# Kernel optimization log

Hardware: AMD Instinct MI355X
Metric: run time of the kernel (lower is better)

The kernel has to match this reference:

```python
import jax, jax.numpy as jnp
import numpy as np

NUM_HEADS = 8

def setup_inputs() -> dict:
    key = jax.random.key(0)
    ks = jax.random.split(key, 9)
    b, s, d = 2, 2048, 512
    e = d * NUM_HEADS  # 4096
    sc = 0.02
    return {
        "x": jax.random.normal(ks[0], (b, s, d), jnp.float32),
        "Wq": jax.random.normal(ks[1], (e, d), jnp.float32) * sc,
        "bq": jax.random.normal(ks[2], (e,), jnp.float32) * sc,
        "Wk": jax.random.normal(ks[3], (e, d), jnp.float32) * sc,
        "bk": jax.random.normal(ks[4], (e,), jnp.float32) * sc,
        "Wv": jax.random.normal(ks[5], (e, d), jnp.float32) * sc,
        "bv": jax.random.normal(ks[6], (e,), jnp.float32) * sc,
        "Wo": jax.random.normal(ks[7], (d, e), jnp.float32) * sc,
        "bo": jax.random.normal(ks[8], (d,), jnp.float32) * sc,
    }

def reference(x, Wq, bq, Wk, bk, Wv, bv, Wo, bo):
    b, s, d = x.shape
    h = NUM_HEADS
    hd = d  # head_dim == model_dimension in this module
    # QKV projections: [b, s, h*hd]
    q = (x @ Wq.T + bq).reshape(b, s, h, hd)
    k = (x @ Wk.T + bk).reshape(b, s, h, hd)
    v = (x @ Wv.T + bv).reshape(b, s, h, hd)
    # scores: [b, h, s_q, s_k]
    scores = jnp.einsum("bqhd,bkhd->bhqk", q, k) / jnp.sqrt(jnp.float32(hd))
    attn = jax.nn.softmax(scores, axis=-1)
    ctx = jnp.einsum("bhqk,bkhd->bqhd", attn, v).reshape(b, s, h * hd)
    return ctx @ Wo.T + bo
```

## Files before the change

kernel.cpp:

```cpp
#include <hip/hip_runtime.h>
#include <hip/hip_bf16.h>

typedef __hip_bfloat16 bf16t;
typedef short bf16x8 __attribute__((ext_vector_type(8)));
typedef float f32x4 __attribute__((ext_vector_type(4)));

__device__ __forceinline__ float b2f(short s) {
    unsigned u = ((unsigned)(unsigned short)s) << 16;
    float f;
    __builtin_memcpy(&f, &u, 4);
    return f;
}

__device__ __forceinline__ unsigned short f2b(float f) {
    unsigned u;
    __builtin_memcpy(&u, &f, 4);
    unsigned r = (u + 0x7fffu + ((u >> 16) & 1u)) >> 16;
    return (unsigned short)r;
}

__device__ __forceinline__ void gload_lds16(const void* g, void* l) {
    __builtin_amdgcn_global_load_lds(
        (const __attribute__((address_space(1))) void*)g,
        (__attribute__((address_space(3))) void*)l,
        16, 0, 0);
}

template<int EPI>
__global__ __launch_bounds__(512, 2)
void gemm8p(const bf16t* __restrict__ Ag, const bf16t* __restrict__ Bg,
            void* __restrict__ Cg, const float* __restrict__ bias,
            float* __restrict__ part,
            int K, int lda, int ldb, int ldc,
            long aOffB, long aOffH, long bOffB, long bOffH,
            long cOffB, long cOffH, float scale)
{
    __shared__ __align__(16) char lds8[131072];

    unsigned gx = gridDim.x, gy = gridDim.y;
    unsigned nwg = gx * gy * gridDim.z;
    unsigned wg = (blockIdx.z * gy + blockIdx.y) * gx + blockIdx.x;
    if ((nwg & 7u) == 0u) wg = (wg & 7u) * (nwg >> 3) + (wg >> 3);
    const unsigned pz = wg / (gx * gy);
    const unsigned prem = wg - pz * gx * gy;
    const unsigned py = prem / gx;
    const unsigned px = prem - py * gx;

    const int zb = pz >> 3, zh = pz & 7;
    const int brow = py * 256;
    const int bcol = px * 256;

    const size_t ldab = (size_t)lda * 2;
    const size_t ldbb = (size_t)ldb * 2;
    const char* Agb = (const char*)(Ag + (size_t)zb * aOffB + (size_t)zh * aOffH)
                      + (size_t)brow * ldab;
    const char* Bgb = (const char*)(Bg + (size_t)zb * bOffB + (size_t)zh * bOffH)
                      + (size_t)bcol * ldbb;

    const int t    = threadIdx.x;
    const int lane = t & 63;
    const int wid  = t >> 6;
    const int wm   = wid >> 2;
    const int wn   = wid & 3;
    const int lr   = lane & 15;
    const int lk   = lane >> 4;

    const int srow = t >> 2;
    const int scg  = (t & 3) ^ ((srow >> 1) & 3);
    const size_t aSrc = (size_t)srow * ldab + (size_t)scg * 16;
    const size_t bSrc = (size_t)srow * ldbb + (size_t)scg * 16;
    const int dst0 = t * 16;
    char* ldsA = lds8;
    char* ldsB = lds8 + 65536;

    const int rchunk = lk ^ ((lr >> 1) & 3);
    const int aByte = (wm * 128 + lr) * 64 + rchunk * 16;
    const int bByte = (wn * 64 + lr) * 64 + rchunk * 16;

    f32x4 acc[8][4];
#pragma unroll
    for (int i = 0; i < 8; ++i)
#pragma unroll
        for (int j = 0; j < 4; ++j)
            acc[i][j] = (f32x4){0.f, 0.f, 0.f, 0.f};

    const int nk = K >> 5;

#define STAGE_A(kt, bufi) do {                                              \
        const char* s_ = Agb + (size_t)(kt) * 64 + aSrc;                    \
        char* d_ = ldsA + (bufi) * 16384 + dst0;                            \
        gload_lds16(s_, d_);                                                \
        gload_lds16(s_ + 128 * ldab, d_ + 8192);                            \
    } while (0)
#define STAGE_B(kt, bufi) do {                                              \
        const char* s_ = Bgb + (size_t)(kt) * 64 + bSrc;                    \
        char* d_ = ldsB + (bufi) * 16384 + dst0;                            \
        gload_lds16(s_, d_);                                                \
        gload_lds16(s_ + 128 * ldbb, d_ + 8192);                            \
    } while (0)

    const int npro = nk < 3 ? nk : 3;
    for (int p = 0; p < npro; ++p) { STAGE_A(p, p & 3); STAGE_B(p, p & 3); }
    if (npro == 3) asm volatile("s_waitcnt vmcnt(8)" ::: "memory");
    else           asm volatile("s_waitcnt vmcnt(0)" ::: "memory");
    __builtin_amdgcn_s_barrier();

    for (int kt = 0; kt < nk; ++kt) {
        const int buf  = kt & 3;
        const int bufS = (kt + 3) & 3;
        const bool st  = (kt + 3) < nk;
        const char* lA = ldsA + buf * 16384;
        const char* lB = ldsB + buf * 16384;

        bf16x8 af[4], bfv[4];
#pragma unroll
        for (int i = 0; i < 4; ++i) af[i]  = *(const bf16x8*)(lA + aByte + i * 1024);
#pragma unroll
        for (int j = 0; j < 4; ++j) bfv[j] = *(const bf16x8*)(lB + bByte + j * 1024);
        if (st) STAGE_A(kt + 3, bufS);
        __builtin_amdgcn_s_setprio(1);
#pragma unroll
        for (int i = 0; i < 4; ++i)
#pragma unroll
            for (int j = 0; j < 4; ++j)
                acc[i][j] = __builtin_amdgcn_mfma_f32_16x16x32_bf16(af[i], bfv[j], acc[i][j], 0, 0, 0);
        __builtin_amdgcn_s_setprio(0);
        asm volatile("" ::: "memory");
        __builtin_amdgcn_s_barrier();

        bf16x8 af2[4];
#pragma unroll
        for (int i = 0; i < 4; ++i) af2[i] = *(const bf16x8*)(lA + aByte + (i + 4) * 1024);
        if (st) STAGE_B(kt + 3, bufS);
        if (st)                  asm volatile("s_waitcnt vmcnt(8)" ::: "memory");
        else if (kt + 2 < nk)    asm volatile("s_waitcnt vmcnt(4)" ::: "memory");
        else if (kt + 1 < nk)    asm volatile("s_waitcnt vmcnt(0)" ::: "memory");
        __builtin_amdgcn_s_setprio(1);
#pragma unroll
        for (int i = 0; i < 4; ++i)
#pragma unroll
            for (int j = 0; j < 4; ++j)
                acc[i + 4][j] = __builtin_amdgcn_mfma_f32_16x16x32_bf16(af2[i], bfv[j], acc[i + 4][j], 0, 0, 0);
        __builtin_amdgcn_s_setprio(0);
        asm volatile("" ::: "memory");
        __builtin_amdgcn_s_barrier();
    }
#undef STAGE_A
#undef STAGE_B

    if (EPI == 4) {
#pragma unroll
        for (int i = 0; i < 8; ++i)
#pragma unroll
            for (int j = 0; j < 4; ++j)
#pragma unroll
                for (int r = 0; r < 4; ++r)
                    acc[i][j][r] = __expf(acc[i][j][r] * scale);
#pragma unroll
        for (int i = 0; i < 8; ++i)
#pragma unroll
            for (int r = 0; r < 4; ++r) {
                float v = acc[i][0][r] + acc[i][1][r] + acc[i][2][r] + acc[i][3][r];
                v += __shfl_xor(v, 1);
                v += __shfl_xor(v, 2);
                v += __shfl_xor(v, 4);
                v += __shfl_xor(v, 8);
                if (lr == 0)
                    part[((size_t)pz * 2048 + brow + wm * 128 + i * 16 + lk * 4 + r) * 32
                         + px * 4 + wn] = v;
            }
        __syncthreads();
        unsigned short* lC = (unsigned short*)lds8;
#pragma unroll
        for (int i = 0; i < 8; ++i)
#pragma unroll
            for (int j = 0; j < 4; ++j) {
                int col = wn * 64 + j * 16 + lr;
#pragma unroll
                for (int r = 0; r < 4; ++r) {
                    int row = wm * 128 + i * 16 + lk * 4 + r;
                    lC[row * 256 + col] = f2b(acc[i][j][r]);
                }
            }
        __syncthreads();
        unsigned short* C = (unsigned short*)((bf16t*)Cg + (size_t)zb * cOffB + (size_t)zh * cOffH);
#pragma unroll
        for (int p = 0; p < 16; ++p) {
            int c  = p * 512 + t;
            int row = c >> 5;
            int cc  = c & 31;
            bf16x8 v = *(const bf16x8*)(lC + (size_t)c * 8);
            *(bf16x8*)(C + (size_t)(brow + row) * ldc + bcol + cc * 8) = v;
        }
    } else if (EPI == 3) {
        __syncthreads();
        float* ldsInv = (float*)lds8;
        if (t < 256) {
            const float* pp = part + ((size_t)pz * 2048 + brow + t) * 32;
            float s = 0.f;
#pragma unroll
            for (int p = 0; p < 32; ++p) s += pp[p];
            ldsInv[t] = 1.0f / s;
        }
        __syncthreads();
        float linv[8][4];
#pragma unroll
        for (int i = 0; i < 8; ++i)
#pragma unroll
            for (int r = 0; r < 4; ++r)
                linv[i][r] = ldsInv[wm * 128 + i * 16 + lk * 4 + r];
        __syncthreads();
        unsigned short* lC = (unsigned short*)lds8;
#pragma unroll
        for (int i = 0; i < 8; ++i)
#pragma unroll
            for (int j = 0; j < 4; ++j) {
                int col = wn * 64 + j * 16 + lr;
#pragma unroll
                for (int r = 0; r < 4; ++r) {
                    int row = wm * 128 + i * 16 + lk * 4 + r;
                    lC[row * 256 + col] = f2b(acc[i][j][r] * linv[i][r]);
                }
            }
        __syncthreads();
        unsigned short* C = (unsigned short*)((bf16t*)Cg + (size_t)zb * cOffB + (size_t)zh * cOffH);
#pragma unroll
        for (int p = 0; p < 16; ++p) {
            int c  = p * 512 + t;
            int row = c >> 5;
            int cc  = c & 31;
            bf16x8 v = *(const bf16x8*)(lC + (size_t)c * 8);
            *(bf16x8*)(C + (size_t)(brow + row) * ldc + bcol + cc * 8) = v;
        }
    } else if (EPI == 0) {
        __syncthreads();
        unsigned short* lC = (unsigned short*)lds8;
#pragma unroll
        for (int i = 0; i < 8; ++i)
#pragma unroll
            for (int j = 0; j < 4; ++j) {
                int col = wn * 64 + j * 16 + lr;
                float badd = bias ? bias[bcol + col] : 0.f;
#pragma unroll
                for (int r = 0; r < 4; ++r) {
                    int row = wm * 128 + i * 16 + lk * 4 + r;
                    lC[row * 256 + col] = f2b(acc[i][j][r] * scale + badd);
                }
            }
        __syncthreads();
        unsigned short* C = (unsigned short*)((bf16t*)Cg + (size_t)zb * cOffB + (size_t)zh * cOffH);
#pragma unroll
        for (int p = 0; p < 16; ++p) {
            int c  = p * 512 + t;
            int row = c >> 5;
            int cc  = c & 31;
            bf16x8 v = *(const bf16x8*)(lC + (size_t)c * 8);
            *(bf16x8*)(C + (size_t)(brow + row) * ldc + bcol + cc * 8) = v;
        }
    } else {
        unsigned short* C = (unsigned short*)Cg;
#pragma unroll
        for (int i = 0; i < 8; ++i)
#pragma unroll
            for (int j = 0; j < 4; ++j) {
                int col = bcol + wn * 64 + j * 16 + lr;
                int hh = col >> 9, dd = col & 511;
                float badd = bias ? bias[col] : 0.f;
                int row0 = brow + wm * 128 + i * 16 + lk * 4;
                int bb = row0 >> 11, ss0 = row0 & 2047;
                ushort4 pack;
                pack.x = f2b(acc[i][j][0] * scale + badd);
                pack.y = f2b(acc[i][j][1] * scale + badd);
                pack.z = f2b(acc[i][j][2] * scale + badd);
                pack.w = f2b(acc[i][j][3] * scale + badd);
                size_t addr = ((((size_t)(bb * 8 + hh)) * 512 + dd) << 11) + (size_t)ss0;
                *(ushort4*)(C + addr) = pack;
            }
    }
}

__global__ __launch_bounds__(256, 3)
void gemm_of32(const bf16t* __restrict__ Ag, const bf16t* __restrict__ Bg,
               float* __restrict__ Cg, const float* __restrict__ bias,
               int K, int lda, int ldb, int ldc)
{
    __shared__ __align__(16) char lds[49152];

    unsigned gx = gridDim.x, gy = gridDim.y;
    unsigned nwg = gx * gy;
    unsigned wg = blockIdx.y * gx + blockIdx.x;
    if ((nwg & 7u) == 0u) wg = (wg & 7u) * (nwg >> 3) + (wg >> 3);
    const unsigned py = wg / gx;
    const unsigned px = wg - py * gx;
    const int brow = py * 128;
    const int bcol = px * 64;

    const int t    = threadIdx.x;
    const int lane = t & 63;
    const int wid  = t >> 6;
    const int wr   = wid >> 1, wc = wid & 1;
    const int lr   = lane & 15;
    const int lk   = lane >> 4;

    const size_t ldab = (size_t)lda * 2;
    const size_t ldbb = (size_t)ldb * 2;
    const char* Agb = (const char*)Ag + (size_t)brow * ldab;
    const char* Bgb = (const char*)Bg + (size_t)bcol * ldbb;

    const int srow = t >> 2;
    const int scg  = (t & 3) ^ ((srow >> 1) & 3);
    const size_t aSrc = (size_t)srow * ldab + (size_t)scg * 16;
    const size_t bSrc = (size_t)srow * ldbb + (size_t)scg * 16;
    char* ldsA = lds;
    char* ldsB = lds + 32768;

    const int rchunk = lk ^ ((lr >> 1) & 3);
    const int aByte = (wr * 64 + lr) * 64 + rchunk * 16;
    const int bByte = (wc * 32 + lr) * 64 + rchunk * 16;

    f32x4 acc[4][2];
#pragma unroll
    for (int i = 0; i < 4; ++i)
#pragma unroll
        for (int j = 0; j < 2; ++j)
            acc[i][j] = (f32x4){0.f, 0.f, 0.f, 0.f};

    const int nk = K >> 5;

#define STAGE_O(kt, bufi) do {                                              \
        const char* sa_ = Agb + (size_t)(kt) * 64 + aSrc;                   \
        gload_lds16(sa_,             ldsA + (bufi) * 8192 + t * 16);        \
        gload_lds16(sa_ + 64 * ldab, ldsA + (bufi) * 8192 + 4096 + t * 16); \
        gload_lds16(Bgb + (size_t)(kt) * 64 + bSrc,                         \
                    ldsB + (bufi) * 4096 + t * 16);                         \
    } while (0)

    for (int p = 0; p < 3; ++p) STAGE_O(p, p);
    asm volatile("s_waitcnt vmcnt(6)" ::: "memory");
    __builtin_amdgcn_s_barrier();

    for (int kt = 0; kt < nk; ++kt) {
        const int buf  = kt & 3;
        const bool st  = (kt + 3) < nk;
        const char* lA = ldsA + buf * 8192;
        const char* lB = ldsB + buf * 4096;

        bf16x8 af[4], bfv[2];
#pragma unroll
        for (int i = 0; i < 4; ++i) af[i]  = *(const bf16x8*)(lA + aByte + i * 1024);
#pragma unroll
        for (int j = 0; j < 2; ++j) bfv[j] = *(const bf16x8*)(lB + bByte + j * 1024);
        if (st) STAGE_O(kt + 3, (kt + 3) & 3);
        if (st)                  asm volatile("s_waitcnt vmcnt(6)" ::: "memory");
        else if (kt + 2 < nk)    asm volatile("s_waitcnt vmcnt(3)" ::: "memory");
        else if (kt + 1 < nk)    asm volatile("s_waitcnt vmcnt(0)" ::: "memory");
        __builtin_amdgcn_s_setprio(1);
#pragma unroll
        for (int i = 0; i < 4; ++i)
#pragma unroll
            for (int j = 0; j < 2; ++j)
                acc[i][j] = __builtin_amdgcn_mfma_f32_16x16x32_bf16(af[i], bfv[j], acc[i][j], 0, 0, 0);
        __builtin_amdgcn_s_setprio(0);
        asm volatile("" ::: "memory");
        __builtin_amdgcn_s_barrier();
    }
#undef STAGE_O

    const int orow = brow + wr * 64;
    const int ocol = bcol + wc * 32;
#pragma unroll
    for (int i = 0; i < 4; ++i)
#pragma unroll
        for (int j = 0; j < 2; ++j) {
            int col = ocol + j * 16 + lr;
            float badd = bias[col];
#pragma unroll
            for (int r = 0; r < 4; ++r) {
                int row = orow + i * 16 + lk * 4 + r;
                Cg[(size_t)row * ldc + col] = acc[i][j][r] + badd;
            }
        }
}

__global__ __launch_bounds__(256)
void cvt5(const float* __restrict__ s0, const float* __restrict__ s1,
          const float* __restrict__ s2, const float* __restrict__ s3,
          const float* __restrict__ s4,
          bf16t* __restrict__ d0, bf16t* __restrict__ d1,
          bf16t* __restrict__ d2, bf16t* __restrict__ d3,
          bf16t* __restrict__ d4)
{
    const float* s;
    bf16t* d;
    switch (blockIdx.y) {
        case 0: s = s0; d = d0; break;
        case 1: s = s1; d = d1; break;
        case 2: s = s2; d = d2; break;
        case 3: s = s3; d = d3; break;
        default: s = s4; d = d4; break;
    }
    int i = blockIdx.x * 256 + threadIdx.x;
    float4 f = ((const float4*)s)[i];
    ushort4 o;
    o.x = f2b(f.x); o.y = f2b(f.y); o.z = f2b(f.z); o.w = f2b(f.w);
    ((ushort4*)d)[i] = o;
}

extern "C" void kernel_launch(void* const* d_in, const int* in_sizes, int n_in,
                              void* d_out, int out_size, void* d_ws, size_t ws_size,
                              hipStream_t stream)
{
    const float* x  = (const float*)d_in[0];
    const float* Wq = (const float*)d_in[1];
    const float* bq = (const float*)d_in[2];
    const float* Wk = (const float*)d_in[3];
    const float* bk = (const float*)d_in[4];
    const float* Wv = (const float*)d_in[5];
    const float* bv = (const float*)d_in[6];
    const float* Wo = (const float*)d_in[7];
    const float* bo = (const float*)d_in[8];

    const int Bn = 2, Sn = 2048, Dn = 512, Hn = 8, En = 4096;
    const int Mn = Bn * Sn;
    const float scl = 0.044194173824159216f;

    bf16t* base = (bf16t*)d_ws;
    size_t off = 0;
    bf16t* Qb  = base + off; off += (size_t)Mn * En;
    bf16t* Kb  = base + off; off += (size_t)Mn * En;
    bf16t* Vt  = base + off; off += (size_t)Mn * En;
    bf16t* Xb  = base + off; off += (size_t)Mn * Dn;
    bf16t* Wqb = base + off; off += (size_t)En * Dn;
    bf16t* Wkb = base + off; off += (size_t)En * Dn;
    bf16t* Wvb = base + off; off += (size_t)En * Dn;
    bf16t* Wob = base + off; off += (size_t)Dn * En;
    float* Pt  = (float*)(base + off); off += (size_t)16 * Sn * 32 * 2;
    bf16t* Sb  = base + off;

    cvt5<<<dim3(2048, 5, 1), 256, 0, stream>>>(x, Wq, Wk, Wv, Wo,
                                               Xb, Wqb, Wkb, Wvb, Wob);

    gemm8p<0><<<dim3(En / 256, Mn / 256, 1), 512, 0, stream>>>(
        Xb, Wqb, Qb, bq, nullptr, Dn, Dn, Dn, En, 0, 0, 0, 0, 0, 0, 1.0f);
    gemm8p<0><<<dim3(En / 256, Mn / 256, 1), 512, 0, stream>>>(
        Xb, Wkb, Kb, bk, nullptr, Dn, Dn, Dn, En, 0, 0, 0, 0, 0, 0, 1.0f);
    gemm8p<2><<<dim3(En / 256, Mn / 256, 1), 512, 0, stream>>>(
        Xb, Wvb, Vt, bv, nullptr, Dn, Dn, Dn, En, 0, 0, 0, 0, 0, 0, 1.0f);

    gemm8p<4><<<dim3(Sn / 256, Sn / 256, 16), 512, 0, stream>>>(
        Qb, Kb, Sb, nullptr, Pt, Dn, En, En, Sn,
        (long)Sn * En, (long)Dn, (long)Sn * En, (long)Dn,
        (long)Hn * Sn * Sn, (long)Sn * Sn, scl);

    gemm8p<3><<<dim3(Dn / 256, Sn / 256, 16), 512, 0, stream>>>(
        Sb, Vt, Qb, nullptr, Pt, Sn, Sn, Sn, En,
        (long)Hn * Sn * Sn, (long)Sn * Sn, (long)Hn * Dn * Sn, (long)Dn * Sn,
        (long)Sn * En, (long)Dn, 1.0f);

    gemm_of32<<<dim3(Dn / 64, Mn / 128, 1), 256, 0, stream>>>(
        Qb, Wob, (float*)d_out, bo, En, En, En, Dn);
}
```

Baseline: 300.0 us.

## Shrink GEMM tile to 128x256 with triple-buffered LDS for higher occupancy

Halves the M dimension of the main GEMM block tile from 256 to 128 and cuts the LDS pipeline from four stages to three, shrinking shared memory from 128KB to 72KB. Launch bounds are raised to allow more blocks per CU. The k-loop is restructured into a single MFMA phase per step with an extra barrier and lgkmcnt wait before compute, and the same barrier is added to the output-projection GEMM. This aims to improve occupancy and latency hiding at the cost of less data reuse per tile, more global traffic on the B operand, and an added barrier per iteration.

```diff
diff --git a/kernel.cpp b/kernel.cpp
--- a/kernel.cpp
+++ b/kernel.cpp
@@ -27,15 +27,15 @@
 }
 
 template<int EPI>
-__global__ __launch_bounds__(512, 2)
-void gemm8p(const bf16t* __restrict__ Ag, const bf16t* __restrict__ Bg,
+__global__ __launch_bounds__(512, 4)
+void gemm3b(const bf16t* __restrict__ Ag, const bf16t* __restrict__ Bg,
             void* __restrict__ Cg, const float* __restrict__ bias,
             float* __restrict__ part,
             int K, int lda, int ldb, int ldc,
             long aOffB, long aOffH, long bOffB, long bOffH,
             long cOffB, long cOffH, float scale)
 {
-    __shared__ __align__(16) char lds8[131072];
+    __shared__ __align__(16) char lds8[73728];
 
     unsigned gx = gridDim.x, gy = gridDim.y;
     unsigned nwg = gx * gy * gridDim.z;
@@ -47,7 +47,7 @@
     const unsigned px = prem - py * gx;
 
     const int zb = pz >> 3, zh = pz & 7;
-    const int brow = py * 256;
+    const int brow = py * 128;
     const int bcol = px * 256;
 
     const size_t ldab = (size_t)lda * 2;
@@ -69,55 +69,58 @@
     const int scg  = (t & 3) ^ ((srow >> 1) & 3);
     const size_t aSrc = (size_t)srow * ldab + (size_t)scg * 16;
     const size_t bSrc = (size_t)srow * ldbb + (size_t)scg * 16;
-    const int dst0 = t * 16;
     char* ldsA = lds8;
-    char* ldsB = lds8 + 65536;
+    char* ldsB = lds8 + 24576;
 
     const int rchunk = lk ^ ((lr >> 1) & 3);
-    const int aByte = (wm * 128 + lr) * 64 + rchunk * 16;
+    const int aByte = (wm * 64 + lr) * 64 + rchunk * 16;
     const int bByte = (wn * 64 + lr) * 64 + rchunk * 16;
 
-    f32x4 acc[8][4];
-#pragma unroll
-    for (int i = 0; i < 8; ++i)
+    f32x4 acc[4][4];
+#pragma unroll
+    for (int i = 0; i < 4; ++i)
 #pragma unroll
         for (int j = 0; j < 4; ++j)
             acc[i][j] = (f32x4){0.f, 0.f, 0.f, 0.f};
 
     const int nk = K >> 5;
 
-#define STAGE_A(kt, bufi) do {                                              \
-        const char* s_ = Agb + (size_t)(kt) * 64 + aSrc;                    \
-        char* d_ = ldsA + (bufi) * 16384 + dst0;                            \
-        gload_lds16(s_, d_);                                                \
-        gload_lds16(s_ + 128 * ldab, d_ + 8192);                            \
+#define STAGE(kt, bufi) do {                                                \
+        const char* sa_ = Agb + (size_t)(kt) * 64 + aSrc;                   \
+        gload_lds16(sa_, ldsA + (bufi) * 8192 + t * 16);                    \
+        const char* sb_ = Bgb + (size_t)(kt) * 64 + bSrc;                   \
+        gload_lds16(sb_,              ldsB + (bufi) * 16384 + t * 16);      \
+        gload_lds16(sb_ + 128 * ldbb, ldsB + (bufi) * 16384 + 8192 + t * 16);\
     } while (0)
-#define STAGE_B(kt, bufi) do {                                              \
-        const char* s_ = Bgb + (size_t)(kt) * 64 + bSrc;                    \
-        char* d_ = ldsB + (bufi) * 16384 + dst0;                            \
-        gload_lds16(s_, d_);                                                \
-        gload_lds16(s_ + 128 * ldbb, d_ + 8192);                            \
-    } while (0)
-
-    const int npro = nk < 3 ? nk : 3;
-    for (int p = 0; p < npro; ++p) { STAGE_A(p, p & 3); STAGE_B(p, p & 3); }
-    if (npro == 3) asm volatile("s_waitcnt vmcnt(8)" ::: "memory");
-    else           asm volatile("s_waitcnt vmcnt(0)" ::: "memory");
+
+    STAGE(0, 0);
+    if (nk > 1) {
+        STAGE(1, 1);
+        asm volatile("s_waitcnt vmcnt(3)" ::: "memory");
+    } else {
+        asm volatile("s_waitcnt vmcnt(0)" ::: "memory");
+    }
     __builtin_amdgcn_s_barrier();
 
+    int bufR = 0, bufS = 2;
     for (int kt = 0; kt < nk; ++kt) {
-        const int buf  = kt & 3;
-        const int bufS = (kt + 3) & 3;
-        const bool st  = (kt + 3) < nk;
-        const char* lA = ldsA + buf * 16384;
-        const char* lB = ldsB + buf * 16384;
+        const char* lA = ldsA + bufR * 8192;
+        const char* lB = ldsB + bufR * 16384;
 
         bf16x8 af[4], bfv[4];
 #pragma unroll
         for (int i = 0; i < 4; ++i) af[i]  = *(const bf16x8*)(lA + aByte + i * 1024);
 #pragma unroll
         for (int j = 0; j < 4; ++j) bfv[j] = *(const bf16x8*)(lB + bByte + j * 1024);
-        if (st) STAGE_A(kt + 3, bufS);
+
+        if (kt + 2 < nk) {
+            STAGE(kt + 2, bufS);
+            asm volatile("s_waitcnt vmcnt(3)" ::: "memory");
+        } else if (kt + 1 < nk) {
+            asm volatile("s_waitcnt vmcnt(0)" ::: "memory");
+        }
+        __builtin_amdgcn_s_barrier();
+        asm volatile("s_waitcnt lgkmcnt(0)" ::: "memory");
         __builtin_amdgcn_s_setprio(1);
 #pragma unroll
         for (int i = 0; i < 4; ++i)
@@ -128,36 +131,21 @@
         asm volatile("" ::: "memory");
         __builtin_amdgcn_s_barrier();
 
-        bf16x8 af2[4];
-#pragma unroll
-        for (int i = 0; i < 4; ++i) af2[i] = *(const bf16x8*)(lA + aByte + (i + 4) * 1024);
-        if (st) STAGE_B(kt + 3, bufS);
-        if (st)                  asm volatile("s_waitcnt vmcnt(8)" ::: "memory");
-        else if (kt + 2 < nk)    asm volatile("s_waitcnt vmcnt(4)" ::: "memory");
-        else if (kt + 1 < nk)    asm volatile("s_waitcnt vmcnt(0)" ::: "memory");
-        __builtin_amdgcn_s_setprio(1);
-#pragma unroll
-        for (int i = 0; i < 4; ++i)
-#pragma unroll
-            for (int j = 0; j < 4; ++j)
-                acc[i + 4][j] = __builtin_amdgcn_mfma_f32_16x16x32_bf16(af2[i], bfv[j], acc[i + 4][j], 0, 0, 0);
-        __builtin_amdgcn_s_setprio(0);
-        asm volatile("" ::: "memory");
-        __builtin_amdgcn_s_barrier();
+        bufR = (bufR == 2) ? 0 : bufR + 1;
+        bufS = (bufS == 2) ? 0 : bufS + 1;
     }
-#undef STAGE_A
-#undef STAGE_B
+#undef STAGE
 
     if (EPI == 4) {
 #pragma unroll
-        for (int i = 0; i < 8; ++i)
+        for (int i = 0; i < 4; ++i)
 #pragma unroll
             for (int j = 0; j < 4; ++j)
 #pragma unroll
                 for (int r = 0; r < 4; ++r)
                     acc[i][j][r] = __expf(acc[i][j][r] * scale);
 #pragma unroll
-        for (int i = 0; i < 8; ++i)
+        for (int i = 0; i < 4; ++i)
 #pragma unroll
             for (int r = 0; r < 4; ++r) {
                 float v = acc[i][0][r] + acc[i][1][r] + acc[i][2][r] + acc[i][3][r];
@@ -166,26 +154,26 @@
                 v += __shfl_xor(v, 4);
                 v += __shfl_xor(v, 8);
                 if (lr == 0)
-                    part[((size_t)pz * 2048 + brow + wm * 128 + i * 16 + lk * 4 + r) * 32
+                    part[((size_t)pz * 2048 + brow + wm * 64 + i * 16 + lk * 4 + r) * 32
                          + px * 4 + wn] = v;
             }
         __syncthreads();
         unsigned short* lC = (unsigned short*)lds8;
 #pragma unroll
-        for (int i = 0; i < 8; ++i)
+        for (int i = 0; i < 4; ++i)
 #pragma unroll
             for (int j = 0; j < 4; ++j) {
                 int col = wn * 64 + j * 16 + lr;
 #pragma unroll
                 for (int r = 0; r < 4; ++r) {
-                    int row = wm * 128 + i * 16 + lk * 4 + r;
+                    int row = wm * 64 + i * 16 + lk * 4 + r;
                     lC[row * 256 + col] = f2b(acc[i][j][r]);
                 }
             }
         __syncthreads();
         unsigned short* C = (unsigned short*)((bf16t*)Cg + (size_t)zb * cOffB + (size_t)zh * cOffH);
 #pragma unroll
-        for (int p = 0; p < 16; ++p) {
+        for (int p = 0; p < 8; ++p) {
             int c  = p * 512 + t;
             int row = c >> 5;
             int cc  = c & 31;
@@ -195,7 +183,7 @@
     } else if (EPI == 3) {
         __syncthreads();
         float* ldsInv = (float*)lds8;
-        if (t < 256) {
+        if (t < 128) {
             const float* pp = part + ((size_t)pz * 2048 + brow + t) * 32;
             float s = 0.f;
 #pragma unroll
@@ -203,29 +191,29 @@
             ldsInv[t] = 1.0f / s;
         }
         __syncthreads();
-        float linv[8][4];
-#pragma unroll
-        for (int i = 0; i < 8; ++i)
+        float linv[4][4];
+#pragma unroll
+        for (int i = 0; i < 4; ++i)
 #pragma unroll
             for (int r = 0; r < 4; ++r)
-                linv[i][r] = ldsInv[wm * 128 + i * 16 + lk * 4 + r];
+                linv[i][r] = ldsInv[wm * 64 + i * 16 + lk * 4 + r];
         __syncthreads();
         unsigned short* lC = (unsigned short*)lds8;
 #pragma unroll
-        for (int i = 0; i < 8; ++i)
+        for (int i = 0; i < 4; ++i)
 #pragma unroll
             for (int j = 0; j < 4; ++j) {
                 int col = wn * 64 + j * 16 + lr;
 #pragma unroll
                 for (int r = 0; r < 4; ++r) {
-                    int row = wm * 128 + i * 16 + lk * 4 + r;
+                    int row = wm * 64 + i * 16 + lk * 4 + r;
                     lC[row * 256 + col] = f2b(acc[i][j][r] * linv[i][r]);
                 }
             }
         __syncthreads();
         unsigned short* C = (unsigned short*)((bf16t*)Cg + (size_t)zb * cOffB + (size_t)zh * cOffH);
 #pragma unroll
-        for (int p = 0; p < 16; ++p) {
+        for (int p = 0; p < 8; ++p) {
             int c  = p * 512 + t;
             int row = c >> 5;
             int cc  = c & 31;
@@ -236,21 +224,21 @@
         __syncthreads();
         unsigned short* lC = (unsigned short*)lds8;
 #pragma unroll
-        for (int i = 0; i < 8; ++i)
+        for (int i = 0; i < 4; ++i)
 #pragma unroll
             for (int j = 0; j < 4; ++j) {
                 int col = wn * 64 + j * 16 + lr;
                 float badd = bias ? bias[bcol + col] : 0.f;
 #pragma unroll
                 for (int r = 0; r < 4; ++r) {
-                    int row = wm * 128 + i * 16 + lk * 4 + r;
+                    int row = wm * 64 + i * 16 + lk * 4 + r;
                     lC[row * 256 + col] = f2b(acc[i][j][r] * scale + badd);
                 }
             }
         __syncthreads();
         unsigned short* C = (unsigned short*)((bf16t*)Cg + (size_t)zb * cOffB + (size_t)zh * cOffH);
 #pragma unroll
-        for (int p = 0; p < 16; ++p) {
+        for (int p = 0; p < 8; ++p) {
             int c  = p * 512 + t;
             int row = c >> 5;
             int cc  = c & 31;
@@ -260,13 +248,13 @@
     } else {
         unsigned short* C = (unsigned short*)Cg;
 #pragma unroll
-        for (int i = 0; i < 8; ++i)
+        for (int i = 0; i < 4; ++i)
 #pragma unroll
             for (int j = 0; j < 4; ++j) {
                 int col = bcol + wn * 64 + j * 16 + lr;
                 int hh = col >> 9, dd = col & 511;
                 float badd = bias ? bias[col] : 0.f;
-                int row0 = brow + wm * 128 + i * 16 + lk * 4;
+                int row0 = brow + wm * 64 + i * 16 + lk * 4;
                 int bb = row0 >> 11, ss0 = row0 & 2047;
                 ushort4 pack;
                 pack.x = f2b(acc[i][j][0] * scale + badd);
@@ -354,6 +342,8 @@
         if (st)                  asm volatile("s_waitcnt vmcnt(6)" ::: "memory");
         else if (kt + 2 < nk)    asm volatile("s_waitcnt vmcnt(3)" ::: "memory");
         else if (kt + 1 < nk)    asm volatile("s_waitcnt vmcnt(0)" ::: "memory");
+        __builtin_amdgcn_s_barrier();
+        asm volatile("s_waitcnt lgkmcnt(0)" ::: "memory");
         __builtin_amdgcn_s_setprio(1);
 #pragma unroll
         for (int i = 0; i < 4; ++i)
@@ -440,19 +430,19 @@
     cvt5<<<dim3(2048, 5, 1), 256, 0, stream>>>(x, Wq, Wk, Wv, Wo,
                                                Xb, Wqb, Wkb, Wvb, Wob);
 
-    gemm8p<0><<<dim3(En / 256, Mn / 256, 1), 512, 0, stream>>>(
+    gemm3b<0><<<dim3(En / 256, Mn / 128, 1), 512, 0, stream>>>(
         Xb, Wqb, Qb, bq, nullptr, Dn, Dn, Dn, En, 0, 0, 0, 0, 0, 0, 1.0f);
-    gemm8p<0><<<dim3(En / 256, Mn / 256, 1), 512, 0, stream>>>(
+    gemm3b<0><<<dim3(En / 256, Mn / 128, 1), 512, 0, stream>>>(
         Xb, Wkb, Kb, bk, nullptr, Dn, Dn, Dn, En, 0, 0, 0, 0, 0, 0, 1.0f);
-    gemm8p<2><<<dim3(En / 256, Mn / 256, 1), 512, 0, stream>>>(
+    gemm3b<2><<<dim3(En / 256, Mn / 128, 1), 512, 0, stream>>>(
         Xb, Wvb, Vt, bv, nullptr, Dn, Dn, Dn, En, 0, 0, 0, 0, 0, 0, 1.0f);
 
-    gemm8p<4><<<dim3(Sn / 256, Sn / 256, 16), 512, 0, stream>>>(
+    gemm3b<4><<<dim3(Sn / 256, Sn / 128, 16), 512, 0, stream>>>(
         Qb, Kb, Sb, nullptr, Pt, Dn, En, En, Sn,
         (long)Sn * En, (long)Dn, (long)Sn * En, (long)Dn,
         (long)Hn * Sn * Sn, (long)Sn * Sn, scl);
 
-    gemm8p<3><<<dim3(Dn / 256, Sn / 256, 16), 512, 0, stream>>>(
+    gemm3b<3><<<dim3(Dn / 256, Sn / 128, 16), 512, 0, stream>>>(
         Sb, Vt, Qb, nullptr, Pt, Sn, Sn, Sn, En,
         (long)Hn * Sn * Sn, (long)Sn * Sn, (long)Hn * Dn * Sn, (long)Dn * Sn,
         (long)Sn * En, (long)Dn, 1.0f);
```

Result: slower. 307.0 us (+2.3%).

## Fuse QKV projections into one GEMM and restage main loop with two-deep prefetch

Applied to the files above, without the earlier changes.

The three separate Q/K/V projection GEMMs are merged into a single launch over a concatenated weight buffer. A new epilogue routes each column block to Q, K or the transposed V layout, and the biases are packed into one buffer by the conversion kernel. The GEMM main loop is restructured to process two k-tiles per iteration with a prefetch distance of two instead of three, adding extra barriers and lgkmcnt waits before each MFMA block. This cuts launch count and improves wave fill for the projection, but the shallower prefetch and extra barriers may expose more memory latency.

```diff
diff --git a/kernel.cpp b/kernel.cpp
--- a/kernel.cpp
+++ b/kernel.cpp
@@ -28,7 +28,7 @@
 
 template<int EPI>
 __global__ __launch_bounds__(512, 2)
-void gemm8p(const bf16t* __restrict__ Ag, const bf16t* __restrict__ Bg,
+void gemm4p(const bf16t* __restrict__ Ag, const bf16t* __restrict__ Bg,
             void* __restrict__ Cg, const float* __restrict__ bias,
             float* __restrict__ part,
             int K, int lda, int ldb, int ldc,
@@ -99,25 +99,31 @@
         gload_lds16(s_ + 128 * ldbb, d_ + 8192);                            \
     } while (0)
 
-    const int npro = nk < 3 ? nk : 3;
-    for (int p = 0; p < npro; ++p) { STAGE_A(p, p & 3); STAGE_B(p, p & 3); }
-    if (npro == 3) asm volatile("s_waitcnt vmcnt(8)" ::: "memory");
-    else           asm volatile("s_waitcnt vmcnt(0)" ::: "memory");
+    STAGE_A(0, 0); STAGE_B(0, 0);
+    STAGE_A(1, 1); STAGE_B(1, 1);
+    asm volatile("s_waitcnt vmcnt(4)" ::: "memory");
     __builtin_amdgcn_s_barrier();
 
-    for (int kt = 0; kt < nk; ++kt) {
-        const int buf  = kt & 3;
-        const int bufS = (kt + 3) & 3;
-        const bool st  = (kt + 3) < nk;
-        const char* lA = ldsA + buf * 16384;
-        const char* lB = ldsB + buf * 16384;
+    const int nh = nk >> 1;
+    for (int J = 0; J < nh; ++J) {
+        const int t0 = 2 * J;
+        const int b0 = t0 & 3, b1 = (t0 + 1) & 3;
+        const int s0 = t0 + 2, s1 = t0 + 3;
+        const bool st = s0 < nk;
+        const int sb0 = s0 & 3, sb1 = s1 & 3;
+        const char* lA0 = ldsA + b0 * 16384;
+        const char* lB0 = ldsB + b0 * 16384;
+        const char* lA1 = ldsA + b1 * 16384;
+        const char* lB1 = ldsB + b1 * 16384;
 
         bf16x8 af[4], bfv[4];
 #pragma unroll
-        for (int i = 0; i < 4; ++i) af[i]  = *(const bf16x8*)(lA + aByte + i * 1024);
-#pragma unroll
-        for (int j = 0; j < 4; ++j) bfv[j] = *(const bf16x8*)(lB + bByte + j * 1024);
-        if (st) STAGE_A(kt + 3, bufS);
+        for (int i = 0; i < 4; ++i) af[i]  = *(const bf16x8*)(lA0 + aByte + i * 1024);
+#pragma unroll
+        for (int j = 0; j < 4; ++j) bfv[j] = *(const bf16x8*)(lB0 + bByte + j * 1024);
+        if (st) STAGE_A(s0, sb0);
+        __builtin_amdgcn_s_barrier();
+        asm volatile("s_waitcnt lgkmcnt(0)" ::: "memory");
         __builtin_amdgcn_s_setprio(1);
 #pragma unroll
         for (int i = 0; i < 4; ++i)
@@ -130,11 +136,45 @@
 
         bf16x8 af2[4];
 #pragma unroll
-        for (int i = 0; i < 4; ++i) af2[i] = *(const bf16x8*)(lA + aByte + (i + 4) * 1024);
-        if (st) STAGE_B(kt + 3, bufS);
-        if (st)                  asm volatile("s_waitcnt vmcnt(8)" ::: "memory");
-        else if (kt + 2 < nk)    asm volatile("s_waitcnt vmcnt(4)" ::: "memory");
-        else if (kt + 1 < nk)    asm volatile("s_waitcnt vmcnt(0)" ::: "memory");
+        for (int i = 0; i < 4; ++i) af2[i] = *(const bf16x8*)(lA0 + aByte + (i + 4) * 1024);
+        if (st) STAGE_B(s0, sb0);
+        if (st) asm volatile("s_waitcnt vmcnt(4)" ::: "memory");
+        else    asm volatile("s_waitcnt vmcnt(0)" ::: "memory");
+        __builtin_amdgcn_s_barrier();
+        asm volatile("s_waitcnt lgkmcnt(0)" ::: "memory");
+        __builtin_amdgcn_s_setprio(1);
+#pragma unroll
+        for (int i = 0; i < 4; ++i)
+#pragma unroll
+            for (int j = 0; j < 4; ++j)
+                acc[i + 4][j] = __builtin_amdgcn_mfma_f32_16x16x32_bf16(af2[i], bfv[j], acc[i + 4][j], 0, 0, 0);
+        __builtin_amdgcn_s_setprio(0);
+        asm volatile("" ::: "memory");
+        __builtin_amdgcn_s_barrier();
+
+#pragma unroll
+        for (int i = 0; i < 4; ++i) af[i]  = *(const bf16x8*)(lA1 + aByte + i * 1024);
+#pragma unroll
+        for (int j = 0; j < 4; ++j) bfv[j] = *(const bf16x8*)(lB1 + bByte + j * 1024);
+        if (st) STAGE_A(s1, sb1);
+        __builtin_amdgcn_s_barrier();
+        asm volatile("s_waitcnt lgkmcnt(0)" ::: "memory");
+        __builtin_amdgcn_s_setprio(1);
+#pragma unroll
+        for (int i = 0; i < 4; ++i)
+#pragma unroll
+            for (int j = 0; j < 4; ++j)
+                acc[i][j] = __builtin_amdgcn_mfma_f32_16x16x32_bf16(af[i], bfv[j], acc[i][j], 0, 0, 0);
+        __builtin_amdgcn_s_setprio(0);
+        asm volatile("" ::: "memory");
+        __builtin_amdgcn_s_barrier();
+
+#pragma unroll
+        for (int i = 0; i < 4; ++i) af2[i] = *(const bf16x8*)(lA1 + aByte + (i + 4) * 1024);
+        if (st) STAGE_B(s1, sb1);
+        if (st) asm volatile("s_waitcnt vmcnt(4)" ::: "memory");
+        __builtin_amdgcn_s_barrier();
+        asm volatile("s_waitcnt lgkmcnt(0)" ::: "memory");
         __builtin_amdgcn_s_setprio(1);
 #pragma unroll
         for (int i = 0; i < 4; ++i)
@@ -232,30 +272,53 @@
             bf16x8 v = *(const bf16x8*)(lC + (size_t)c * 8);
             *(bf16x8*)(C + (size_t)(brow + row) * ldc + bcol + cc * 8) = v;
         }
-    } else if (EPI == 0) {
-        __syncthreads();
-        unsigned short* lC = (unsigned short*)lds8;
-#pragma unroll
-        for (int i = 0; i < 8; ++i)
-#pragma unroll
-            for (int j = 0; j < 4; ++j) {
-                int col = wn * 64 + j * 16 + lr;
-                float badd = bias ? bias[bcol + col] : 0.f;
-#pragma unroll
-                for (int r = 0; r < 4; ++r) {
-                    int row = wm * 128 + i * 16 + lk * 4 + r;
-                    lC[row * 256 + col] = f2b(acc[i][j][r] * scale + badd);
+    } else if (EPI == 5) {
+        const int sel = bcol >> 12;
+        const int colw0 = bcol & 4095;
+        if (sel < 2) {
+            __syncthreads();
+            unsigned short* lC = (unsigned short*)lds8;
+#pragma unroll
+            for (int i = 0; i < 8; ++i)
+#pragma unroll
+                for (int j = 0; j < 4; ++j) {
+                    int col = wn * 64 + j * 16 + lr;
+                    float badd = bias[bcol + col];
+#pragma unroll
+                    for (int r = 0; r < 4; ++r) {
+                        int row = wm * 128 + i * 16 + lk * 4 + r;
+                        lC[row * 256 + col] = f2b(acc[i][j][r] + badd);
+                    }
                 }
+            __syncthreads();
+            unsigned short* C = (unsigned short*)((bf16t*)Cg + (size_t)sel * cOffB);
+#pragma unroll
+            for (int p = 0; p < 16; ++p) {
+                int c  = p * 512 + t;
+                int row = c >> 5;
+                int cc  = c & 31;
+                bf16x8 v = *(const bf16x8*)(lC + (size_t)c * 8);
+                *(bf16x8*)(C + (size_t)(brow + row) * ldc + colw0 + cc * 8) = v;
             }
-        __syncthreads();
-        unsigned short* C = (unsigned short*)((bf16t*)Cg + (size_t)zb * cOffB + (size_t)zh * cOffH);
-#pragma unroll
-        for (int p = 0; p < 16; ++p) {
-            int c  = p * 512 + t;
-            int row = c >> 5;
-            int cc  = c & 31;
-            bf16x8 v = *(const bf16x8*)(lC + (size_t)c * 8);
-            *(bf16x8*)(C + (size_t)(brow + row) * ldc + bcol + cc * 8) = v;
+        } else {
+            unsigned short* C = (unsigned short*)part;
+#pragma unroll
+            for (int i = 0; i < 8; ++i)
+#pragma unroll
+                for (int j = 0; j < 4; ++j) {
+                    int col = colw0 + wn * 64 + j * 16 + lr;
+                    int hh = col >> 9, dd = col & 511;
+                    float badd = bias[8192 + col];
+                    int row0 = brow + wm * 128 + i * 16 + lk * 4;
+                    int bb = row0 >> 11, ss0 = row0 & 2047;
+                    ushort4 pack;
+                    pack.x = f2b(acc[i][j][0] + badd);
+                    pack.y = f2b(acc[i][j][1] + badd);
+                    pack.z = f2b(acc[i][j][2] + badd);
+                    pack.w = f2b(acc[i][j][3] + badd);
+                    size_t addr = ((((size_t)(bb * 8 + hh)) * 512 + dd) << 11) + (size_t)ss0;
+                    *(ushort4*)(C + addr) = pack;
+                }
         }
     } else {
         unsigned short* C = (unsigned short*)Cg;
@@ -354,6 +417,8 @@
         if (st)                  asm volatile("s_waitcnt vmcnt(6)" ::: "memory");
         else if (kt + 2 < nk)    asm volatile("s_waitcnt vmcnt(3)" ::: "memory");
         else if (kt + 1 < nk)    asm volatile("s_waitcnt vmcnt(0)" ::: "memory");
+        __builtin_amdgcn_s_barrier();
+        asm volatile("s_waitcnt lgkmcnt(0)" ::: "memory");
         __builtin_amdgcn_s_setprio(1);
 #pragma unroll
         for (int i = 0; i < 4; ++i)
@@ -383,13 +448,25 @@
 }
 
 __global__ __launch_bounds__(256)
-void cvt5(const float* __restrict__ s0, const float* __restrict__ s1,
+void cvt6(const float* __restrict__ s0, const float* __restrict__ s1,
           const float* __restrict__ s2, const float* __restrict__ s3,
           const float* __restrict__ s4,
           bf16t* __restrict__ d0, bf16t* __restrict__ d1,
           bf16t* __restrict__ d2, bf16t* __restrict__ d3,
-          bf16t* __restrict__ d4)
+          bf16t* __restrict__ d4,
+          const float* __restrict__ bq, const float* __restrict__ bk,
+          const float* __restrict__ bv, float* __restrict__ bqkv)
 {
+    int i = blockIdx.x * 256 + threadIdx.x;
+    if (blockIdx.y == 5) {
+        if (i < 3072) {
+            int e = i * 4;
+            const float* src = (e < 4096) ? (bq + e) : (e < 8192) ? (bk + e - 4096) : (bv + e - 8192);
+            float4 f = *(const float4*)src;
+            *(float4*)(bqkv + e) = f;
+        }
+        return;
+    }
     const float* s;
     bf16t* d;
     switch (blockIdx.y) {
@@ -399,7 +476,6 @@
         case 3: s = s3; d = d3; break;
         default: s = s4; d = d4; break;
     }
-    int i = blockIdx.x * 256 + threadIdx.x;
     float4 f = ((const float4*)s)[i];
     ushort4 o;
     o.x = f2b(f.x); o.y = f2b(f.y); o.z = f2b(f.z); o.w = f2b(f.w);
@@ -430,29 +506,27 @@
     bf16t* Kb  = base + off; off += (size_t)Mn * En;
     bf16t* Vt  = base + off; off += (size_t)Mn * En;
     bf16t* Xb  = base + off; off += (size_t)Mn * Dn;
-    bf16t* Wqb = base + off; off += (size_t)En * Dn;
-    bf16t* Wkb = base + off; off += (size_t)En * Dn;
-    bf16t* Wvb = base + off; off += (size_t)En * Dn;
+    bf16t* Wc  = base + off; off += (size_t)3 * En * Dn;
     bf16t* Wob = base + off; off += (size_t)Dn * En;
+    float* Pbias = (float*)(base + off); off += 12288;
     float* Pt  = (float*)(base + off); off += (size_t)16 * Sn * 32 * 2;
     bf16t* Sb  = base + off;
 
-    cvt5<<<dim3(2048, 5, 1), 256, 0, stream>>>(x, Wq, Wk, Wv, Wo,
-                                               Xb, Wqb, Wkb, Wvb, Wob);
-
-    gemm8p<0><<<dim3(En / 256, Mn / 256, 1), 512, 0, stream>>>(
-        Xb, Wqb, Qb, bq, nullptr, Dn, Dn, Dn, En, 0, 0, 0, 0, 0, 0, 1.0f);
-    gemm8p<0><<<dim3(En / 256, Mn / 256, 1), 512, 0, stream>>>(
-        Xb, Wkb, Kb, bk, nullptr, Dn, Dn, Dn, En, 0, 0, 0, 0, 0, 0, 1.0f);
-    gemm8p<2><<<dim3(En / 256, Mn / 256, 1), 512, 0, stream>>>(
-        Xb, Wvb, Vt, bv, nullptr, Dn, Dn, Dn, En, 0, 0, 0, 0, 0, 0, 1.0f);
-
-    gemm8p<4><<<dim3(Sn / 256, Sn / 256, 16), 512, 0, stream>>>(
+    cvt6<<<dim3(2048, 6, 1), 256, 0, stream>>>(
+        x, Wq, Wk, Wv, Wo,
+        Xb, Wc, Wc + (size_t)En * Dn, Wc + (size_t)2 * En * Dn, Wob,
+        bq, bk, bv, Pbias);
+
+    gemm4p<5><<<dim3(3 * En / 256, Mn / 256, 1), 512, 0, stream>>>(
+        Xb, Wc, Qb, Pbias, (float*)Vt, Dn, Dn, Dn, En,
+        0, 0, 0, 0, (long)Mn * En, 0, 1.0f);
+
+    gemm4p<4><<<dim3(Sn / 256, Sn / 256, 16), 512, 0, stream>>>(
         Qb, Kb, Sb, nullptr, Pt, Dn, En, En, Sn,
         (long)Sn * En, (long)Dn, (long)Sn * En, (long)Dn,
         (long)Hn * Sn * Sn, (long)Sn * Sn, scl);
 
-    gemm8p<3><<<dim3(Dn / 256, Sn / 256, 16), 512, 0, stream>>>(
+    gemm4p<3><<<dim3(Dn / 256, Sn / 256, 16), 512, 0, stream>>>(
         Sb, Vt, Qb, nullptr, Pt, Sn, Sn, Sn, En,
         (long)Hn * Sn * Sn, (long)Sn * Sn, (long)Hn * Dn * Sn, (long)Dn * Sn,
         (long)Sn * En, (long)Dn, 1.0f);
```

New measurement: 296.7 us. Within noise of the previous version (-1.1%).

## Fuse Q/K/V projections into one GEMM launch and add pre-MFMA barriers

Applied to the files above, without the earlier changes.

Concatenates the bf16 Wq/Wk/Wv weights and their biases during conversion so that a single GEMM launch with a new epilogue computes all three projections. Column blocks are routed to Q, K (row-major through LDS) or transposed V depending on block column. This removes two kernel launches and the tail effects of three small grids. Separately, it inserts an s_barrier plus lgkmcnt(0) wait before each MFMA block in both GEMM main loops. These add synchronization that could cost throughput, or could act as a correctness/scheduling fix.

```diff
diff --git a/kernel.cpp b/kernel.cpp
--- a/kernel.cpp
+++ b/kernel.cpp
@@ -118,6 +118,8 @@
 #pragma unroll
         for (int j = 0; j < 4; ++j) bfv[j] = *(const bf16x8*)(lB + bByte + j * 1024);
         if (st) STAGE_A(kt + 3, bufS);
+        __builtin_amdgcn_s_barrier();
+        asm volatile("s_waitcnt lgkmcnt(0)" ::: "memory");
         __builtin_amdgcn_s_setprio(1);
 #pragma unroll
         for (int i = 0; i < 4; ++i)
@@ -135,6 +137,8 @@
         if (st)                  asm volatile("s_waitcnt vmcnt(8)" ::: "memory");
         else if (kt + 2 < nk)    asm volatile("s_waitcnt vmcnt(4)" ::: "memory");
         else if (kt + 1 < nk)    asm volatile("s_waitcnt vmcnt(0)" ::: "memory");
+        __builtin_amdgcn_s_barrier();
+        asm volatile("s_waitcnt lgkmcnt(0)" ::: "memory");
         __builtin_amdgcn_s_setprio(1);
 #pragma unroll
         for (int i = 0; i < 4; ++i)
@@ -232,30 +236,53 @@
             bf16x8 v = *(const bf16x8*)(lC + (size_t)c * 8);
             *(bf16x8*)(C + (size_t)(brow + row) * ldc + bcol + cc * 8) = v;
         }
-    } else if (EPI == 0) {
-        __syncthreads();
-        unsigned short* lC = (unsigned short*)lds8;
-#pragma unroll
-        for (int i = 0; i < 8; ++i)
-#pragma unroll
-            for (int j = 0; j < 4; ++j) {
-                int col = wn * 64 + j * 16 + lr;
-                float badd = bias ? bias[bcol + col] : 0.f;
-#pragma unroll
-                for (int r = 0; r < 4; ++r) {
-                    int row = wm * 128 + i * 16 + lk * 4 + r;
-                    lC[row * 256 + col] = f2b(acc[i][j][r] * scale + badd);
+    } else if (EPI == 5) {
+        const int sel = bcol >> 12;
+        const int colw0 = bcol & 4095;
+        if (sel < 2) {
+            __syncthreads();
+            unsigned short* lC = (unsigned short*)lds8;
+#pragma unroll
+            for (int i = 0; i < 8; ++i)
+#pragma unroll
+                for (int j = 0; j < 4; ++j) {
+                    int col = wn * 64 + j * 16 + lr;
+                    float badd = bias[bcol + col];
+#pragma unroll
+                    for (int r = 0; r < 4; ++r) {
+                        int row = wm * 128 + i * 16 + lk * 4 + r;
+                        lC[row * 256 + col] = f2b(acc[i][j][r] + badd);
+                    }
                 }
+            __syncthreads();
+            unsigned short* C = (unsigned short*)((bf16t*)Cg + (size_t)sel * cOffB);
+#pragma unroll
+            for (int p = 0; p < 16; ++p) {
+                int c  = p * 512 + t;
+                int row = c >> 5;
+                int cc  = c & 31;
+                bf16x8 v = *(const bf16x8*)(lC + (size_t)c * 8);
+                *(bf16x8*)(C + (size_t)(brow + row) * ldc + colw0 + cc * 8) = v;
             }
-        __syncthreads();
-        unsigned short* C = (unsigned short*)((bf16t*)Cg + (size_t)zb * cOffB + (size_t)zh * cOffH);
-#pragma unroll
-        for (int p = 0; p < 16; ++p) {
-            int c  = p * 512 + t;
-            int row = c >> 5;
-            int cc  = c & 31;
-            bf16x8 v = *(const bf16x8*)(lC + (size_t)c * 8);
-            *(bf16x8*)(C + (size_t)(brow + row) * ldc + bcol + cc * 8) = v;
+        } else {
+            unsigned short* C = (unsigned short*)part;
+#pragma unroll
+            for (int i = 0; i < 8; ++i)
+#pragma unroll
+                for (int j = 0; j < 4; ++j) {
+                    int col = colw0 + wn * 64 + j * 16 + lr;
+                    int hh = col >> 9, dd = col & 511;
+                    float badd = bias[8192 + col];
+                    int row0 = brow + wm * 128 + i * 16 + lk * 4;
+                    int bb = row0 >> 11, ss0 = row0 & 2047;
+                    ushort4 pack;
+                    pack.x = f2b(acc[i][j][0] + badd);
+                    pack.y = f2b(acc[i][j][1] + badd);
+                    pack.z = f2b(acc[i][j][2] + badd);
+                    pack.w = f2b(acc[i][j][3] + badd);
+                    size_t addr = ((((size_t)(bb * 8 + hh)) * 512 + dd) << 11) + (size_t)ss0;
+                    *(ushort4*)(C + addr) = pack;
+                }
         }
     } else {
         unsigned short* C = (unsigned short*)Cg;
@@ -354,6 +381,8 @@
         if (st)                  asm volatile("s_waitcnt vmcnt(6)" ::: "memory");
         else if (kt + 2 < nk)    asm volatile("s_waitcnt vmcnt(3)" ::: "memory");
         else if (kt + 1 < nk)    asm volatile("s_waitcnt vmcnt(0)" ::: "memory");
+        __builtin_amdgcn_s_barrier();
+        asm volatile("s_waitcnt lgkmcnt(0)" ::: "memory");
         __builtin_amdgcn_s_setprio(1);
 #pragma unroll
         for (int i = 0; i < 4; ++i)
@@ -383,13 +412,25 @@
 }
 
 __global__ __launch_bounds__(256)
-void cvt5(const float* __restrict__ s0, const float* __restrict__ s1,
+void cvt6(const float* __restrict__ s0, const float* __restrict__ s1,
           const float* __restrict__ s2, const float* __restrict__ s3,
           const float* __restrict__ s4,
           bf16t* __restrict__ d0, bf16t* __restrict__ d1,
           bf16t* __restrict__ d2, bf16t* __restrict__ d3,
-          bf16t* __restrict__ d4)
+          bf16t* __restrict__ d4,
+          const float* __restrict__ bq, const float* __restrict__ bk,
+          const float* __restrict__ bv, float* __restrict__ bqkv)
 {
+    int i = blockIdx.x * 256 + threadIdx.x;
+    if (blockIdx.y == 5) {
+        if (i < 3072) {
+            int e = i * 4;
+            const float* src = (e < 4096) ? (bq + e) : (e < 8192) ? (bk + e - 4096) : (bv + e - 8192);
+            float4 f = *(const float4*)src;
+            *(float4*)(bqkv + e) = f;
+        }
+        return;
+    }
     const float* s;
     bf16t* d;
     switch (blockIdx.y) {
@@ -399,7 +440,6 @@
         case 3: s = s3; d = d3; break;
         default: s = s4; d = d4; break;
     }
-    int i = blockIdx.x * 256 + threadIdx.x;
     float4 f = ((const float4*)s)[i];
     ushort4 o;
     o.x = f2b(f.x); o.y = f2b(f.y); o.z = f2b(f.z); o.w = f2b(f.w);
@@ -430,22 +470,20 @@
     bf16t* Kb  = base + off; off += (size_t)Mn * En;
     bf16t* Vt  = base + off; off += (size_t)Mn * En;
     bf16t* Xb  = base + off; off += (size_t)Mn * Dn;
-    bf16t* Wqb = base + off; off += (size_t)En * Dn;
-    bf16t* Wkb = base + off; off += (size_t)En * Dn;
-    bf16t* Wvb = base + off; off += (size_t)En * Dn;
+    bf16t* Wc  = base + off; off += (size_t)3 * En * Dn;
     bf16t* Wob = base + off; off += (size_t)Dn * En;
+    float* Pbias = (float*)(base + off); off += 12288;
     float* Pt  = (float*)(base + off); off += (size_t)16 * Sn * 32 * 2;
     bf16t* Sb  = base + off;
 
-    cvt5<<<dim3(2048, 5, 1), 256, 0, stream>>>(x, Wq, Wk, Wv, Wo,
-                                               Xb, Wqb, Wkb, Wvb, Wob);
-
-    gemm8p<0><<<dim3(En / 256, Mn / 256, 1), 512, 0, stream>>>(
-        Xb, Wqb, Qb, bq, nullptr, Dn, Dn, Dn, En, 0, 0, 0, 0, 0, 0, 1.0f);
-    gemm8p<0><<<dim3(En / 256, Mn / 256, 1), 512, 0, stream>>>(
-        Xb, Wkb, Kb, bk, nullptr, Dn, Dn, Dn, En, 0, 0, 0, 0, 0, 0, 1.0f);
-    gemm8p<2><<<dim3(En / 256, Mn / 256, 1), 512, 0, stream>>>(
-        Xb, Wvb, Vt, bv, nullptr, Dn, Dn, Dn, En, 0, 0, 0, 0, 0, 0, 1.0f);
+    cvt6<<<dim3(2048, 6, 1), 256, 0, stream>>>(
+        x, Wq, Wk, Wv, Wo,
+        Xb, Wc, Wc + (size_t)En * Dn, Wc + (size_t)2 * En * Dn, Wob,
+        bq, bk, bv, Pbias);
+
+    gemm8p<5><<<dim3(3 * En / 256, Mn / 256, 1), 512, 0, stream>>>(
+        Xb, Wc, Qb, Pbias, (float*)Vt, Dn, Dn, Dn, En,
+        0, 0, 0, 0, (long)Mn * En, 0, 1.0f);
 
     gemm8p<4><<<dim3(Sn / 256, Sn / 256, 16), 512, 0, stream>>>(
         Qb, Kb, Sb, nullptr, Pt, Dn, En, En, Sn,
```

Result: no change. 303.7 us (+1.2%).
